# Kernel optimization log

Hardware: AMD Instinct MI355X
Metric: run time of the kernel (lower is better)

The kernel has to match this reference:

```python
import jax, jax.numpy as jnp
import numpy as np

RADIUS = 0.5
NEG_INF = -jnp.inf


def setup_inputs() -> dict:
    key = jax.random.key(0)
    ks = jax.random.split(key, 10)
    N_q, N_o, pos_dim, latent_dim = 2048, 2048, 3, 64
    enc_dim = 3 * pos_dim  # q_pos, o_pos, rel
    inp = {
        "h_obs": jax.random.normal(ks[0], (N_o, latent_dim), dtype=jnp.float32),
        "x_obs": jax.random.normal(ks[1], (N_o, latent_dim), dtype=jnp.float32),
        "pos_obs": jax.random.uniform(ks[2], (N_o, pos_dim), dtype=jnp.float32),
        "pos_query": jax.random.uniform(ks[3], (N_q, pos_dim), dtype=jnp.float32),
        # kernel_mlp: Linear(enc_dim->latent) + ReLU + Linear(latent->1)
        "W1": jax.random.normal(ks[4], (enc_dim, latent_dim), dtype=jnp.float32) / np.sqrt(enc_dim),
        "b1": jnp.zeros((latent_dim,), dtype=jnp.float32),
        "W2": jax.random.normal(ks[5], (latent_dim, 1), dtype=jnp.float32) / np.sqrt(latent_dim),
        "b2": jnp.zeros((1,), dtype=jnp.float32),
        # value_proj: Linear(latent->latent)
        "Wv": jax.random.normal(ks[6], (latent_dim, latent_dim), dtype=jnp.float32) / np.sqrt(latent_dim),
        "bv": jnp.zeros((latent_dim,), dtype=jnp.float32),
    }
    return inp


def reference(h_obs, x_obs, pos_obs, pos_query, W1, b1, W2, b2, Wv, bv):
    # rel: [N_q, N_o, pos_dim]
    rel = pos_query[:, None, :] - pos_obs[None, :, :]
    N_q, N_o, _ = rel.shape
    pos_q_exp = jnp.broadcast_to(pos_query[:, None, :], rel.shape)
    pos_o_exp = jnp.broadcast_to(pos_obs[None, :, :], rel.shape)
    kernel_input = jnp.concatenate([pos_q_exp, pos_o_exp, rel], axis=-1)  # [N_q, N_o, 3*pos_dim]
    # small pointwise MLP over all pairs
    hidden = jax.nn.relu(jnp.einsum('qoe,el->qol', kernel_input, W1) + b1)  # [N_q, N_o, latent]
    logits = jnp.einsum('qol,lk->qok', hidden, W2)[..., 0] + b2[0]          # [N_q, N_o]
    # radius mask
    dist = jnp.linalg.norm(rel, axis=-1)
    logits = jnp.where(dist > RADIUS, NEG_INF, logits)
    # softmax over observations (dim=1)
    weights = jax.nn.softmax(logits, axis=1)  # [N_q, N_o]
    v = h_obs @ Wv + bv                        # [N_o, latent]
    h_query = weights @ v                      # [N_q, latent]
    return h_query
```

## Files before the change

kernel.cpp:

```cpp
#include <hip/hip_runtime.h>

#define NQ 2048
#define NO 2048
#define NOC 16

constexpr size_t OFF_P = 0;
constexpr size_t P_ROW = 68;
constexpr size_t OFF_V = (size_t)NOC * NQ * P_ROW;

__global__ __launch_bounds__(256, 2) void gano_prep(
    const float* __restrict__ h_obs,
    const float* __restrict__ Wv,
    float* __restrict__ ws)
{
    __shared__ __align__(16) float wv[64 * 64];
    const int tid  = threadIdx.x;
    const int lane = tid & 63;
    const int wave = tid >> 6;
    {
        const float4* src = (const float4*)Wv;
        float4* dst = (float4*)wv;
#pragma unroll
        for (int k = 0; k < 4; ++k) dst[tid + k * 256] = src[tid + k * 256];
    }
    __syncthreads();
    const int o = blockIdx.x * 4 + wave;
    const float4* hp = (const float4*)(h_obs + (size_t)o * 64);
    float a0 = 0.f, a1 = 0.f, a2 = 0.f, a3 = 0.f;
#pragma unroll
    for (int kb = 0; kb < 16; ++kb) {
        float4 h4 = hp[kb];
        a0 += h4.x * wv[(kb * 4 + 0) * 64 + lane];
        a1 += h4.y * wv[(kb * 4 + 1) * 64 + lane];
        a2 += h4.z * wv[(kb * 4 + 2) * 64 + lane];
        a3 += h4.w * wv[(kb * 4 + 3) * 64 + lane];
    }
    ws[OFF_V + (size_t)o * 64 + lane] = (a0 + a1) + (a2 + a3);
}

__global__ __launch_bounds__(256, 2) void gano_main(
    const float* __restrict__ ws,
    const float* __restrict__ pos_obs,
    const float* __restrict__ pos_query,
    const float* __restrict__ W1,
    const float* __restrict__ b1,
    const float* __restrict__ W2,
    float* __restrict__ P)
{
    __shared__ __align__(16) float tl[64 * 68];
    __shared__ float po[3 * 64];
    __shared__ float w1q[3 * 64];
    __shared__ float w1o[3 * 64];
    __shared__ float b1l[64];
    __shared__ __align__(16) float w2l[64];

    const int tid  = threadIdx.x;
    const int lane = tid & 63;
    const int wave = tid >> 6;
    const int qg = blockIdx.x >> 4;
    const int oc = blockIdx.x & 15;
    const int q  = qg * 64 + lane;

    if (tid < 64) {
        float w6 = W1[6 * 64 + tid], w7 = W1[7 * 64 + tid], w8 = W1[8 * 64 + tid];
        w1q[0 * 64 + tid] = W1[0 * 64 + tid] + w6;
        w1q[1 * 64 + tid] = W1[1 * 64 + tid] + w7;
        w1q[2 * 64 + tid] = W1[2 * 64 + tid] + w8;
        w1o[0 * 64 + tid] = W1[3 * 64 + tid] - w6;
        w1o[1 * 64 + tid] = W1[4 * 64 + tid] - w7;
        w1o[2 * 64 + tid] = W1[5 * 64 + tid] - w8;
        b1l[tid] = b1[tid];
        w2l[tid] = W2[tid];
    }
    float pq0 = pos_query[q * 3 + 0];
    float pq1 = pos_query[q * 3 + 1];
    float pq2 = pos_query[q * 3 + 2];
    __syncthreads();

    float u[64];
#pragma unroll
    for (int l = 0; l < 64; ++l)
        u[l] = b1l[l] + pq0 * w1q[l] + pq1 * w1q[64 + l] + pq2 * w1q[128 + l];

    float h[64];
#pragma unroll
    for (int l = 0; l < 64; ++l) h[l] = 0.f;
    float s = 0.f;
    const int ow = wave * 16;

    for (int ot = 0; ot < 2; ++ot) {
        const int obase = oc * 128 + ot * 64;
        float po0 = pos_obs[(obase + lane) * 3 + 0];
        float po1 = pos_obs[(obase + lane) * 3 + 1];
        float po2 = pos_obs[(obase + lane) * 3 + 2];
        if (wave == 0) { po[lane] = po0; po[64 + lane] = po1; po[128 + lane] = po2; }
#pragma unroll
        for (int j = 0; j < 16; ++j) {
            int l = wave * 16 + j;
            tl[l * 68 + lane] = po0 * w1o[l] + po1 * w1o[64 + l] + po2 * w1o[128 + l];
        }
        __syncthreads();

        float lg[16];
#pragma unroll
        for (int o = 0; o < 16; ++o) lg[o] = 0.f;
#pragma unroll
        for (int lb = 0; lb < 16; ++lb) {
            float4 wv = *(const float4*)(w2l + lb * 4);
#pragma unroll
            for (int dl = 0; dl < 4; ++dl) {
                const int l = lb * 4 + dl;
                const float4* tr = (const float4*)(tl + l * 68 + ow);
                float ul = u[l];
                float wl = (dl == 0) ? wv.x : (dl == 1) ? wv.y : (dl == 2) ? wv.z : wv.w;
#pragma unroll
                for (int j = 0; j < 4; ++j) {
                    float4 t4 = tr[j];
                    lg[4 * j + 0] += wl * fmaxf(ul + t4.x, 0.f);
                    lg[4 * j + 1] += wl * fmaxf(ul + t4.y, 0.f);
                    lg[4 * j + 2] += wl * fmaxf(ul + t4.z, 0.f);
                    lg[4 * j + 3] += wl * fmaxf(ul + t4.w, 0.f);
                }
            }
        }
        float e[16];
#pragma unroll
        for (int o = 0; o < 16; ++o) {
            float d0 = pq0 - po[ow + o];
            float d1 = pq1 - po[64 + ow + o];
            float d2 = pq2 - po[128 + ow + o];
            float dd = d0 * d0 + d1 * d1 + d2 * d2;
            float ev = (dd > 0.25f) ? 0.f : __expf(lg[o]);
            e[o] = ev; s += ev;
        }
        __syncthreads();

        {
            const float4* src = (const float4*)(ws + OFF_V + (size_t)obase * 64);
            float4* dst = (float4*)tl;
#pragma unroll
            for (int k = 0; k < 4; ++k) dst[tid + k * 256] = src[tid + k * 256];
        }
        __syncthreads();

#pragma unroll
        for (int o = 0; o < 16; ++o) {
            float ev = e[o];
            const float4* vr = (const float4*)(tl + (ow + o) * 64);
#pragma unroll
            for (int j = 0; j < 16; ++j) {
                float4 v4 = vr[j];
                h[4 * j + 0] += ev * v4.x;
                h[4 * j + 1] += ev * v4.y;
                h[4 * j + 2] += ev * v4.z;
                h[4 * j + 3] += ev * v4.w;
            }
        }
        __syncthreads();
    }

    for (int r = 1; r <= 3; ++r) {
        if (wave == r) {
#pragma unroll
            for (int l = 0; l < 64; ++l) tl[l * 65 + lane] = h[l];
            tl[64 * 65 + lane] = s;
        }
        __syncthreads();
        if (wave == 0) {
#pragma unroll
            for (int l = 0; l < 64; ++l) h[l] += tl[l * 65 + lane];
            s += tl[64 * 65 + lane];
        }
        __syncthreads();
    }
    if (wave == 0) {
#pragma unroll
        for (int l = 0; l < 64; ++l) tl[l * 65 + lane] = h[l];
        tl[64 * 65 + lane] = s;
    }
    __syncthreads();

    {
        float* base = P + ((size_t)oc * NQ + (size_t)qg * 64) * P_ROW;
#pragma unroll
        for (int k = 0; k < 17; ++k) {
            int idx = k * 256 + tid;
            int qloc = idx / 68, j = idx % 68;
            float v = 0.f;
            if (j < 65) v = tl[j * 65 + qloc];
            base[idx] = v;
        }
    }
}

__global__ __launch_bounds__(256) void gano_comb(
    const float* __restrict__ P,
    const float* __restrict__ bv,
    float* __restrict__ out)
{
    const int tid = threadIdx.x;
    const int l = tid & 63;
    const int qi = tid >> 6;
    const int q = blockIdx.x * 4 + qi;
    float hs = 0.f, ss = 0.f;
#pragma unroll
    for (int c = 0; c < NOC; ++c) {
        const float* row = P + ((size_t)c * NQ + q) * P_ROW;
        hs += row[l];
        ss += row[64];
    }
    out[(size_t)q * 64 + l] = hs / ss + bv[l];
}

extern "C" void kernel_launch(void* const* d_in, const int* in_sizes, int n_in,
                              void* d_out, int out_size, void* d_ws, size_t ws_size,
                              hipStream_t stream) {
    const float* h_obs     = (const float*)d_in[0];
    const float* pos_obs   = (const float*)d_in[2];
    const float* pos_query = (const float*)d_in[3];
    const float* W1        = (const float*)d_in[4];
    const float* b1        = (const float*)d_in[5];
    const float* W2        = (const float*)d_in[6];
    const float* Wv        = (const float*)d_in[8];
    const float* bv        = (const float*)d_in[9];
    float* ws  = (float*)d_ws;
    float* out = (float*)d_out;

    gano_prep<<<dim3(NO / 4), dim3(256), 0, stream>>>(h_obs, Wv, ws);
    gano_main<<<dim3(512), dim3(256), 0, stream>>>(ws, pos_obs, pos_query, W1, b1, W2, ws + OFF_P);
    gano_comb<<<dim3(NQ / 4), dim3(256), 0, stream>>>(ws + OFF_P, bv, out);
}
```

Measured before the change: 121.9 us.

## Split observations into 32 chunks and partition value accumulation across waves by latent column

The main kernel now gives each block a single 64-observation chunk, with 32 chunks and 1024 blocks. The per-query hidden bias vector moves from 64 registers into LDS. Instead of each wave keeping all 64 latent accumulators for its 16 observations and reducing across waves through LDS, exp weights go to LDS and each wave accumulates 16 latent columns over all 64 observations, reading V directly from global memory. This cuts register pressure so the launch bound can rise to 4 blocks per CU, and it drops the serial cross-wave reduction; V is staged in the output buffer. The cost is a larger partial-result buffer (32 chunks × 64 floats per query) for the combine kernel to write and read.

```diff
diff --git a/kernel.cpp b/kernel.cpp
--- a/kernel.cpp
+++ b/kernel.cpp
@@ -2,16 +2,15 @@
 
 #define NQ 2048
 #define NO 2048
-#define NOC 16
-
-constexpr size_t OFF_P = 0;
-constexpr size_t P_ROW = 68;
-constexpr size_t OFF_V = (size_t)NOC * NQ * P_ROW;
+#define NOC 32
+
+constexpr size_t OFF_PH = 0;
+constexpr size_t OFF_PS = (size_t)NOC * NQ * 64;
 
 __global__ __launch_bounds__(256, 2) void gano_prep(
     const float* __restrict__ h_obs,
     const float* __restrict__ Wv,
-    float* __restrict__ ws)
+    float* __restrict__ V)
 {
     __shared__ __align__(16) float wv[64 * 64];
     const int tid  = threadIdx.x;
@@ -35,31 +34,35 @@
         a2 += h4.z * wv[(kb * 4 + 2) * 64 + lane];
         a3 += h4.w * wv[(kb * 4 + 3) * 64 + lane];
     }
-    ws[OFF_V + (size_t)o * 64 + lane] = (a0 + a1) + (a2 + a3);
-}
-
-__global__ __launch_bounds__(256, 2) void gano_main(
-    const float* __restrict__ ws,
+    V[(size_t)o * 64 + lane] = (a0 + a1) + (a2 + a3);
+}
+
+__global__ __launch_bounds__(256, 4) void gano_main(
+    const float* __restrict__ V,
     const float* __restrict__ pos_obs,
     const float* __restrict__ pos_query,
     const float* __restrict__ W1,
     const float* __restrict__ b1,
     const float* __restrict__ W2,
-    float* __restrict__ P)
+    float* __restrict__ Ph,
+    float* __restrict__ Ps)
 {
     __shared__ __align__(16) float tl[64 * 68];
-    __shared__ float po[3 * 64];
+    __shared__ __align__(16) float ue[16 * 64 * 4];
     __shared__ float w1q[3 * 64];
     __shared__ float w1o[3 * 64];
     __shared__ float b1l[64];
     __shared__ __align__(16) float w2l[64];
+    __shared__ float po[3 * 64];
+    __shared__ float sbuf[4 * 64];
 
     const int tid  = threadIdx.x;
     const int lane = tid & 63;
-    const int wave = tid >> 6;
-    const int qg = blockIdx.x >> 4;
-    const int oc = blockIdx.x & 15;
-    const int q  = qg * 64 + lane;
+    const int wave = __builtin_amdgcn_readfirstlane(tid >> 6);
+    const int qg = blockIdx.x >> 5;
+    const int oc = blockIdx.x & 31;
+    const int obase = oc * 64;
+    const int q = qg * 64 + lane;
 
     if (tid < 64) {
         float w6 = W1[6 * 64 + tid], w7 = W1[7 * 64 + tid], w8 = W1[8 * 64 + tid];
@@ -75,126 +78,100 @@
     float pq0 = pos_query[q * 3 + 0];
     float pq1 = pos_query[q * 3 + 1];
     float pq2 = pos_query[q * 3 + 2];
-    __syncthreads();
-
-    float u[64];
-#pragma unroll
-    for (int l = 0; l < 64; ++l)
-        u[l] = b1l[l] + pq0 * w1q[l] + pq1 * w1q[64 + l] + pq2 * w1q[128 + l];
-
-    float h[64];
-#pragma unroll
-    for (int l = 0; l < 64; ++l) h[l] = 0.f;
-    float s = 0.f;
+    float po0 = pos_obs[(obase + lane) * 3 + 0];
+    float po1 = pos_obs[(obase + lane) * 3 + 1];
+    float po2 = pos_obs[(obase + lane) * 3 + 2];
+    if (wave == 0) { po[lane] = po0; po[64 + lane] = po1; po[128 + lane] = po2; }
+    __syncthreads();
+
+#pragma unroll
+    for (int j = 0; j < 16; ++j) {
+        int l = wave * 16 + j;
+        tl[l * 68 + lane] = po0 * w1o[l] + po1 * w1o[64 + l] + po2 * w1o[128 + l];
+    }
+#pragma unroll
+    for (int k = 0; k < 4; ++k) {
+        int lb = wave * 4 + k;
+        float4 uv;
+        {
+            int l = lb * 4;
+            uv.x = b1l[l+0] + pq0 * w1q[l+0] + pq1 * w1q[64 + l+0] + pq2 * w1q[128 + l+0];
+            uv.y = b1l[l+1] + pq0 * w1q[l+1] + pq1 * w1q[64 + l+1] + pq2 * w1q[128 + l+1];
+            uv.z = b1l[l+2] + pq0 * w1q[l+2] + pq1 * w1q[64 + l+2] + pq2 * w1q[128 + l+2];
+            uv.w = b1l[l+3] + pq0 * w1q[l+3] + pq1 * w1q[64 + l+3] + pq2 * w1q[128 + l+3];
+        }
+        *(float4*)(ue + (size_t)(lb * 64 + lane) * 4) = uv;
+    }
+    __syncthreads();
+
+    float lg[16];
+#pragma unroll
+    for (int o = 0; o < 16; ++o) lg[o] = 0.f;
     const int ow = wave * 16;
-
-    for (int ot = 0; ot < 2; ++ot) {
-        const int obase = oc * 128 + ot * 64;
-        float po0 = pos_obs[(obase + lane) * 3 + 0];
-        float po1 = pos_obs[(obase + lane) * 3 + 1];
-        float po2 = pos_obs[(obase + lane) * 3 + 2];
-        if (wave == 0) { po[lane] = po0; po[64 + lane] = po1; po[128 + lane] = po2; }
-#pragma unroll
-        for (int j = 0; j < 16; ++j) {
-            int l = wave * 16 + j;
-            tl[l * 68 + lane] = po0 * w1o[l] + po1 * w1o[64 + l] + po2 * w1o[128 + l];
-        }
-        __syncthreads();
-
-        float lg[16];
-#pragma unroll
-        for (int o = 0; o < 16; ++o) lg[o] = 0.f;
-#pragma unroll
-        for (int lb = 0; lb < 16; ++lb) {
-            float4 wv = *(const float4*)(w2l + lb * 4);
-#pragma unroll
-            for (int dl = 0; dl < 4; ++dl) {
-                const int l = lb * 4 + dl;
-                const float4* tr = (const float4*)(tl + l * 68 + ow);
-                float ul = u[l];
-                float wl = (dl == 0) ? wv.x : (dl == 1) ? wv.y : (dl == 2) ? wv.z : wv.w;
-#pragma unroll
-                for (int j = 0; j < 4; ++j) {
-                    float4 t4 = tr[j];
-                    lg[4 * j + 0] += wl * fmaxf(ul + t4.x, 0.f);
-                    lg[4 * j + 1] += wl * fmaxf(ul + t4.y, 0.f);
-                    lg[4 * j + 2] += wl * fmaxf(ul + t4.z, 0.f);
-                    lg[4 * j + 3] += wl * fmaxf(ul + t4.w, 0.f);
-                }
+#pragma unroll
+    for (int lb = 0; lb < 16; ++lb) {
+        float4 u4 = *(const float4*)(ue + (size_t)(lb * 64 + lane) * 4);
+        float4 w4 = *(const float4*)(w2l + lb * 4);
+#pragma unroll
+        for (int dl = 0; dl < 4; ++dl) {
+            const int l = lb * 4 + dl;
+            const float4* tr = (const float4*)(tl + l * 68 + ow);
+            float ul = (dl == 0) ? u4.x : (dl == 1) ? u4.y : (dl == 2) ? u4.z : u4.w;
+            float wl = (dl == 0) ? w4.x : (dl == 1) ? w4.y : (dl == 2) ? w4.z : w4.w;
+#pragma unroll
+            for (int j = 0; j < 4; ++j) {
+                float4 t4 = tr[j];
+                lg[4 * j + 0] += wl * fmaxf(ul + t4.x, 0.f);
+                lg[4 * j + 1] += wl * fmaxf(ul + t4.y, 0.f);
+                lg[4 * j + 2] += wl * fmaxf(ul + t4.z, 0.f);
+                lg[4 * j + 3] += wl * fmaxf(ul + t4.w, 0.f);
             }
         }
-        float e[16];
-#pragma unroll
-        for (int o = 0; o < 16; ++o) {
-            float d0 = pq0 - po[ow + o];
-            float d1 = pq1 - po[64 + ow + o];
-            float d2 = pq2 - po[128 + ow + o];
-            float dd = d0 * d0 + d1 * d1 + d2 * d2;
-            float ev = (dd > 0.25f) ? 0.f : __expf(lg[o]);
-            e[o] = ev; s += ev;
-        }
-        __syncthreads();
-
-        {
-            const float4* src = (const float4*)(ws + OFF_V + (size_t)obase * 64);
-            float4* dst = (float4*)tl;
-#pragma unroll
-            for (int k = 0; k < 4; ++k) dst[tid + k * 256] = src[tid + k * 256];
-        }
-        __syncthreads();
-
-#pragma unroll
-        for (int o = 0; o < 16; ++o) {
-            float ev = e[o];
-            const float4* vr = (const float4*)(tl + (ow + o) * 64);
-#pragma unroll
-            for (int j = 0; j < 16; ++j) {
-                float4 v4 = vr[j];
-                h[4 * j + 0] += ev * v4.x;
-                h[4 * j + 1] += ev * v4.y;
-                h[4 * j + 2] += ev * v4.z;
-                h[4 * j + 3] += ev * v4.w;
-            }
-        }
-        __syncthreads();
-    }
-
-    for (int r = 1; r <= 3; ++r) {
-        if (wave == r) {
-#pragma unroll
-            for (int l = 0; l < 64; ++l) tl[l * 65 + lane] = h[l];
-            tl[64 * 65 + lane] = s;
-        }
-        __syncthreads();
-        if (wave == 0) {
-#pragma unroll
-            for (int l = 0; l < 64; ++l) h[l] += tl[l * 65 + lane];
-            s += tl[64 * 65 + lane];
-        }
-        __syncthreads();
-    }
+    }
+    float e[16], spart = 0.f;
+#pragma unroll
+    for (int o = 0; o < 16; ++o) {
+        float d0 = pq0 - po[ow + o];
+        float d1 = pq1 - po[64 + ow + o];
+        float d2 = pq2 - po[128 + ow + o];
+        float dd = d0 * d0 + d1 * d1 + d2 * d2;
+        float ev = (dd > 0.25f) ? 0.f : __expf(lg[o]);
+        e[o] = ev; spart += ev;
+    }
+    __syncthreads();
+#pragma unroll
+    for (int o = 0; o < 16; ++o) ue[(size_t)(ow + o) * 64 + lane] = e[o];
+    sbuf[wave * 64 + lane] = spart;
+    __syncthreads();
+
+    float h0 = 0.f, h1 = 0.f, h2 = 0.f, h3 = 0.f, h4 = 0.f, h5 = 0.f, h6 = 0.f, h7 = 0.f;
+    float h8 = 0.f, h9 = 0.f, hA = 0.f, hB = 0.f, hC = 0.f, hD = 0.f, hE = 0.f, hF = 0.f;
+    const float* vb = V + (size_t)obase * 64 + ow;
+#pragma unroll 4
+    for (int o = 0; o < 64; ++o) {
+        float eo = ue[(size_t)o * 64 + lane];
+        const float4* vr = (const float4*)(vb + (size_t)o * 64);
+        float4 v0 = vr[0], v1 = vr[1], v2 = vr[2], v3 = vr[3];
+        h0 += eo * v0.x; h1 += eo * v0.y; h2 += eo * v0.z; h3 += eo * v0.w;
+        h4 += eo * v1.x; h5 += eo * v1.y; h6 += eo * v1.z; h7 += eo * v1.w;
+        h8 += eo * v2.x; h9 += eo * v2.y; hA += eo * v2.z; hB += eo * v2.w;
+        hC += eo * v3.x; hD += eo * v3.y; hE += eo * v3.z; hF += eo * v3.w;
+    }
+
+    float* hp = Ph + ((size_t)oc * NQ + (size_t)qg * 64 + lane) * 64 + ow;
+    ((float4*)hp)[0] = make_float4(h0, h1, h2, h3);
+    ((float4*)hp)[1] = make_float4(h4, h5, h6, h7);
+    ((float4*)hp)[2] = make_float4(h8, h9, hA, hB);
+    ((float4*)hp)[3] = make_float4(hC, hD, hE, hF);
     if (wave == 0) {
-#pragma unroll
-        for (int l = 0; l < 64; ++l) tl[l * 65 + lane] = h[l];
-        tl[64 * 65 + lane] = s;
-    }
-    __syncthreads();
-
-    {
-        float* base = P + ((size_t)oc * NQ + (size_t)qg * 64) * P_ROW;
-#pragma unroll
-        for (int k = 0; k < 17; ++k) {
-            int idx = k * 256 + tid;
-            int qloc = idx / 68, j = idx % 68;
-            float v = 0.f;
-            if (j < 65) v = tl[j * 65 + qloc];
-            base[idx] = v;
-        }
+        float s = sbuf[lane] + sbuf[64 + lane] + sbuf[128 + lane] + sbuf[192 + lane];
+        Ps[(size_t)oc * NQ + (size_t)qg * 64 + lane] = s;
     }
 }
 
 __global__ __launch_bounds__(256) void gano_comb(
-    const float* __restrict__ P,
+    const float* __restrict__ Ph,
+    const float* __restrict__ Ps,
     const float* __restrict__ bv,
     float* __restrict__ out)
 {
@@ -205,9 +182,8 @@
     float hs = 0.f, ss = 0.f;
 #pragma unroll
     for (int c = 0; c < NOC; ++c) {
-        const float* row = P + ((size_t)c * NQ + q) * P_ROW;
-        hs += row[l];
-        ss += row[64];
+        hs += Ph[((size_t)c * NQ + q) * 64 + l];
+        ss += Ps[(size_t)c * NQ + q];
     }
     out[(size_t)q * 64 + l] = hs / ss + bv[l];
 }
@@ -226,7 +202,8 @@
     float* ws  = (float*)d_ws;
     float* out = (float*)d_out;
 
-    gano_prep<<<dim3(NO / 4), dim3(256), 0, stream>>>(h_obs, Wv, ws);
-    gano_main<<<dim3(512), dim3(256), 0, stream>>>(ws, pos_obs, pos_query, W1, b1, W2, ws + OFF_P);
-    gano_comb<<<dim3(NQ / 4), dim3(256), 0, stream>>>(ws + OFF_P, bv, out);
-}
+    gano_prep<<<dim3(NO / 4), dim3(256), 0, stream>>>(h_obs, Wv, out);
+    gano_main<<<dim3(1024), dim3(256), 0, stream>>>(out, pos_obs, pos_query, W1, b1, W2,
+                                                    ws + OFF_PH, ws + OFF_PS);
+    gano_comb<<<dim3(NQ / 4), dim3(256), 0, stream>>>(ws + OFF_PH, ws + OFF_PS, bv, out);
+}
```

New measurement: 109.0 us. 10.6% less time.
